# Kernel optimization log

Hardware: AMD Instinct MI355X
Metric: run time of the kernel (lower is better)

Reference implementation:

```python
import math
import jax, jax.numpy as jnp
import numpy as np

B, T, I, H = 32, 64, 256, 512
TAU = 20.0                      # tau_trace and membrane tau
DECAY = math.exp(-1.0 / TAU)    # exp trace decay (exp_convolve)
ALPHA = math.exp(-1.0 / TAU)    # leaky-integrator membrane decay
ETA = 0.1                       # Hebbian plasticity learning rate


def setup_inputs() -> dict:
    key = jax.random.key(0)
    kx, kw = jax.random.split(key)
    x = jax.random.normal(kx, (B, T, I), dtype=jnp.float32)
    # xavier_uniform with gain sqrt(2) ~ normal with matched std
    std = math.sqrt(2.0) * math.sqrt(2.0 / (2 * H + I))
    W = (jax.random.normal(kw, (2 * H, I), dtype=jnp.float32) * std)
    return {"x": x, "W": W}


def reference(x, W):
    """Write-mode (recall=False) forward of MemoryLayer.
    Returns (mem [B,H,H], keys [B,T,H], vals [B,T,H])."""
    h = W.shape[0] // 2
    b = x.shape[0]
    # i = linear(x, W): [B,T,2H], split into key/value drives
    i = jnp.einsum('bti,hi->bth', x, W)
    ik, iv = i[..., :h], i[..., h:]

    mem0 = jnp.zeros((b, h, h), x.dtype)
    z = jnp.zeros((b, h), x.dtype)

    def step(carry, inp):
        kv, vv, kt, vt, mem = carry
        ik_t, iv_t = inp
        # key neuron dynamics: leaky integration + tanh
        kv = ALPHA * kv + ik_t
        k = jnp.tanh(kv)
        # associative read: (key.unsqueeze(1) * mem).sum(2) == mem @ key
        ikv = 0.2 * jnp.einsum('bij,bj->bi', mem, k)
        # value neuron dynamics
        vv = ALPHA * vv + iv_t + ikv
        v = jnp.tanh(vv)
        # exp_convolve traces
        kt = DECAY * kt + (1.0 - DECAY) * k
        vt = DECAY * vt + (1.0 - DECAY) * v
        # Hebbian outer-product plasticity: delta_mem = eta * vt (x) kt
        mem = mem + ETA * jnp.einsum('bi,bj->bij', vt, kt)
        return (kv, vv, kt, vt, mem), (k, v)

    # scan over time (sequential recurrence), batch fully vectorized
    (kv, vv, kt, vt, mem), (ks, vs) = jax.lax.scan(
        step, (z, z, z, z, mem0),
        (jnp.swapaxes(ik, 0, 1), jnp.swapaxes(iv, 0, 1)))
    keys = jnp.swapaxes(ks, 0, 1)  # [B,T,H]
    vals = jnp.swapaxes(vs, 0, 1)  # [B,T,H]
    return mem, keys, vals
```

## Files before the change

kernel.cpp:

```cpp
#include <hip/hip_runtime.h>

#define B_ 32
#define T_ 64
#define I_ 256
#define H_ 512

static constexpr float ALPHA_F = 0.951229424500714f;
static constexpr float OMD_F   = 0.048770575499286f;
static constexpr float ETA_F   = 0.1f;
static constexpr float CSCALE  = 0.02f;

typedef __bf16 bf16x8 __attribute__((ext_vector_type(8)));
typedef float  f32x4  __attribute__((ext_vector_type(4)));

__device__ __forceinline__ float tanh_fast(float x) {
  float xc = fminf(fmaxf(x, -15.f), 15.f);
  float e = __expf(2.f * xc);
  return (e - 1.f) * __builtin_amdgcn_rcpf(e + 1.f);
}
__device__ __forceinline__ unsigned int f2bf(float f) {
  unsigned int u = __float_as_uint(f);
  u += 0x7fffu + ((u >> 16) & 1u);
  return u >> 16;
}
__device__ __forceinline__ void split8(const float* p, bf16x8& hi, bf16x8& lo) {
  float4 f0 = *reinterpret_cast<const float4*>(p);
  float4 f1 = *reinterpret_cast<const float4*>(p + 4);
  float f[8] = {f0.x, f0.y, f0.z, f0.w, f1.x, f1.y, f1.z, f1.w};
#pragma unroll
  for (int i = 0; i < 8; ++i) {
    __bf16 h = (__bf16)f[i];
    hi[i] = h;
    lo[i] = (__bf16)(f[i] - (float)h);
  }
}

template <int CTRL>
__device__ __forceinline__ float dpp_add(float x) {
  int mv = __builtin_amdgcn_update_dpp(0, __float_as_int(x), CTRL, 0xF, 0xF, true);
  return x + __int_as_float(mv);
}
__device__ __forceinline__ float wave_sum_dpp(float x) {
  x = dpp_add<0x111>(x);
  x = dpp_add<0x112>(x);
  x = dpp_add<0x114>(x);
  x = dpp_add<0x118>(x);
  x = dpp_add<0x142>(x);
  x = dpp_add<0x143>(x);
  return x;
}

__global__ __launch_bounds__(256) void proj_kscan(const float* __restrict__ x,
                                                  const float* __restrict__ W,
                                                  float* __restrict__ keys,
                                                  float* __restrict__ ktg,
                                                  ushort* __restrict__ ktb16T,
                                                  float* __restrict__ ivbuf) {
  __shared__ float scr[64][68];
  const int b  = blockIdx.x;
  const int n0 = blockIdx.y * 64;
  const int m0 = b * 64;
  const int tid = threadIdx.x;
  const int w = tid >> 6, l = tid & 63;
  const int lrow = l & 15, lk8 = (l >> 4) * 8;

  const float* xr = x + (size_t)(m0 + w * 16 + lrow) * I_ + lk8;
  const float* wr = W + (size_t)(n0 + lrow) * I_ + lk8;
  f32x4 acc[4] = {};
#pragma unroll
  for (int ks = 0; ks < 8; ++ks) {
    bf16x8 ah, al;
    split8(xr + ks * 32, ah, al);
#pragma unroll
    for (int jt = 0; jt < 4; ++jt) {
      bf16x8 bh, bl;
      split8(wr + (size_t)jt * 16 * I_ + ks * 32, bh, bl);
      acc[jt] = __builtin_amdgcn_mfma_f32_16x16x32_bf16(ah, bh, acc[jt], 0, 0, 0);
      acc[jt] = __builtin_amdgcn_mfma_f32_16x16x32_bf16(al, bh, acc[jt], 0, 0, 0);
      acc[jt] = __builtin_amdgcn_mfma_f32_16x16x32_bf16(ah, bl, acc[jt], 0, 0, 0);
    }
  }
  const int tr0 = (l >> 4) * 4, tc = lrow;

  if (n0 < 512) {
#pragma unroll
    for (int jt = 0; jt < 4; ++jt)
#pragma unroll
      for (int r = 0; r < 4; ++r)
        scr[w * 16 + tr0 + r][jt * 16 + tc] = acc[jt][r];
    __syncthreads();
    if (tid < 64) {
      float kv = 0.f, kt = 0.f;
      unsigned int kpk[32];
      float* ko  = keys + (size_t)b * T_ * H_ + n0 + tid;
      float* kto = ktg  + (size_t)b * T_ * H_ + n0 + tid;
#pragma unroll
      for (int t = 0; t < T_; ++t) {
        kv = ALPHA_F * kv + scr[t][tid];
        float k = tanh_fast(kv);
        kt = ALPHA_F * kt + OMD_F * k;
        ko[(size_t)t * H_]  = k;
        kto[(size_t)t * H_] = kt;
        unsigned int us = f2bf(kt);
        if ((t & 1) == 0) kpk[t >> 1] = us;
        else              kpk[t >> 1] |= us << 16;
      }
      ushort* kb = ktb16T + ((size_t)b * H_ + n0 + tid) * T_;
#pragma unroll
      for (int e = 0; e < 8; ++e)
        reinterpret_cast<uint4*>(kb)[e] =
            make_uint4(kpk[4 * e], kpk[4 * e + 1], kpk[4 * e + 2], kpk[4 * e + 3]);
    }
  } else {
    const int hv0 = n0 - 512;
#pragma unroll
    for (int jt = 0; jt < 4; ++jt)
#pragma unroll
      for (int r = 0; r < 4; ++r)
        ivbuf[((size_t)b * T_ + w * 16 + tr0 + r) * H_ + hv0 + jt * 16 + tc] = acc[jt][r];
  }
}

__global__ __launch_bounds__(512) void dots_kernel(const float* __restrict__ keys,
                                                   const float* __restrict__ ktg,
                                                   float* __restrict__ C) {
  const int b = blockIdx.y;
  const int t = blockIdx.x * 8 + (threadIdx.x >> 6);
  const int lane = threadIdx.x & 63;
  const float* krow = keys + ((size_t)b * T_ + t) * H_ + 4 * lane;
  float4 k0 = *reinterpret_cast<const float4*>(krow);
  float4 k1 = *reinterpret_cast<const float4*>(krow + 256);
  const float* tb = ktg + (size_t)b * T_ * H_ + 4 * lane;
  float* Cb = C + ((size_t)b * T_ + t) * T_;
#pragma unroll 8
  for (int s = 0; s < T_; ++s) {
    const float* ar = tb + (size_t)s * H_;
    float4 a0 = *reinterpret_cast<const float4*>(ar);
    float4 a1 = *reinterpret_cast<const float4*>(ar + 256);
    float p = a0.x * k0.x + a0.y * k0.y + a0.z * k0.z + a0.w * k0.w
            + a1.x * k1.x + a1.y * k1.y + a1.z * k1.z + a1.w * k1.w;
    p = wave_sum_dpp(p);
    if (lane == 63) Cb[s] = CSCALE * p;
  }
}

#define IVG(T) (((T) & 3) == 0 ? ivq[(T) >> 2].x : ((T) & 3) == 1 ? ivq[(T) >> 2].y \
              : ((T) & 3) == 2 ? ivq[(T) >> 2].z : ivq[(T) >> 2].w)
#define VQSET(T, val) do { \
    if (((T) & 3) == 0)      vqv[(T) >> 2].x = (val); \
    else if (((T) & 3) == 1) vqv[(T) >> 2].y = (val); \
    else if (((T) & 3) == 2) vqv[(T) >> 2].z = (val); \
    else                     vqv[(T) >> 2].w = (val); } while (0)

#define VSTEP(TT, CUR, NXT)                                                   \
  {                                                                           \
    if ((TT) + 1 < T_) {                                                      \
      _Pragma("unroll")                                                       \
      for (int q = 0; q < 16; ++q)                                            \
        NXT[q] = *reinterpret_cast<const float4*>(&Cs[(TT) + 1][4 * q]);      \
    }                                                                         \
    float p0 = 0.f, p1 = 0.f, p2 = 0.f, p3 = 0.f;                             \
    _Pragma("unroll")                                                         \
    for (int q = 0; q < 16; ++q) {                                            \
      p0 += CUR[q].x * vqv[q].x;                                              \
      p1 += CUR[q].y * vqv[q].y;                                              \
      p2 += CUR[q].z * vqv[q].z;                                              \
      p3 += CUR[q].w * vqv[q].w;                                              \
    }                                                                         \
    float ikv = (p0 + p1) + (p2 + p3);                                        \
    vv = ALPHA_F * vv + IVG(TT) + ikv;                                        \
    float v = tanh_fast(vv);                                                  \
    vt = ALPHA_F * vt + OMD_F * v;                                            \
    VQSET(TT, vt);                                                            \
    vo[(size_t)(TT) * H_] = v;                                                \
  }

#define VP2(T2) VSTEP(T2, ca, cbuf) VSTEP((T2) + 1, cbuf, ca)
#define VP8(T8) VP2(T8) VP2((T8) + 2) VP2((T8) + 4) VP2((T8) + 6)
#define IVLD(Q) { ivq[Q].x = pv[(size_t)(4 * (Q) + 0) * H_]; \
                  ivq[Q].y = pv[(size_t)(4 * (Q) + 1) * H_]; \
                  ivq[Q].z = pv[(size_t)(4 * (Q) + 2) * H_]; \
                  ivq[Q].w = pv[(size_t)(4 * (Q) + 3) * H_]; }

__global__ __launch_bounds__(64, 1) void vscan_kernel(const float* __restrict__ ivbuf,
                                                      const float* __restrict__ C,
                                                      float* __restrict__ vals,
                                                      ushort* __restrict__ vtb16T) {
  __shared__ float Cs[T_][T_];
  const int b    = blockIdx.x >> 3;
  const int lane = threadIdx.x;
  const int h    = ((blockIdx.x & 7) << 6) + lane;

  const float* Cb = C + (size_t)b * T_ * T_;
#pragma unroll
  for (int e = 0; e < 16; ++e)
    reinterpret_cast<float4*>(&Cs[0][0])[lane + (e << 6)] =
        reinterpret_cast<const float4*>(Cb)[lane + (e << 6)];

  const float* pv = ivbuf + (size_t)b * T_ * H_ + h;
  float* vo = vals + ((size_t)b * T_) * H_ + h;

  float4 ivq[16];
  IVLD(0)  IVLD(1)  IVLD(2)  IVLD(3)  IVLD(4)  IVLD(5)  IVLD(6)  IVLD(7)
  IVLD(8)  IVLD(9)  IVLD(10) IVLD(11) IVLD(12) IVLD(13) IVLD(14) IVLD(15)

  float vv = 0.f, vt = 0.f;
  float4 vqv[16];
#pragma unroll
  for (int q = 0; q < 16; ++q) vqv[q] = make_float4(0.f, 0.f, 0.f, 0.f);

  __syncthreads();

  float4 ca[16], cbuf[16];
#pragma unroll
  for (int q = 0; q < 16; ++q)
    ca[q] = *reinterpret_cast<const float4*>(&Cs[0][4 * q]);

  VP8(0) VP8(8) VP8(16) VP8(24) VP8(32) VP8(40) VP8(48) VP8(56)

  ushort* vb16 = vtb16T + ((size_t)b * H_ + h) * T_;
#pragma unroll
  for (int q = 0; q < 16; ++q) {
    unsigned int u0 = f2bf(vqv[q].x) | (f2bf(vqv[q].y) << 16);
    unsigned int u1 = f2bf(vqv[q].z) | (f2bf(vqv[q].w) << 16);
    reinterpret_cast<uint2*>(vb16)[q] = make_uint2(u0, u1);
  }
}

__global__ __launch_bounds__(256) void mem_mfma(const ushort* __restrict__ vtb16T,
                                                const ushort* __restrict__ ktb16T,
                                                float* __restrict__ mem) {
  const int b  = blockIdx.z;
  const int i0 = blockIdx.y * 64;
  const int j0 = blockIdx.x * 64;
  const int tid = threadIdx.x;
  const int w = tid >> 6, l = tid & 63;
  const int lrow = l & 15, lk8 = (l >> 4) * 8;

  const ushort* ar = vtb16T + ((size_t)b * H_ + i0 + w * 16 + lrow) * T_ + lk8;
  const ushort* br = ktb16T + ((size_t)b * H_ + j0 + lrow) * T_ + lk8;
  f32x4 acc[4] = {};
#pragma unroll
  for (int ks = 0; ks < 2; ++ks) {
    bf16x8 a = *reinterpret_cast<const bf16x8*>(ar + ks * 32);
#pragma unroll
    for (int jt = 0; jt < 4; ++jt) {
      bf16x8 bv = *reinterpret_cast<const bf16x8*>(br + (size_t)jt * 16 * T_ + ks * 32);
      acc[jt] = __builtin_amdgcn_mfma_f32_16x16x32_bf16(a, bv, acc[jt], 0, 0, 0);
    }
  }
  const int tr0 = (l >> 4) * 4, tc = lrow;
  float* mb = mem + (size_t)b * H_ * H_;
#pragma unroll
  for (int jt = 0; jt < 4; ++jt)
#pragma unroll
    for (int r = 0; r < 4; ++r)
      mb[((size_t)i0 + w * 16 + tr0 + r) * H_ + j0 + jt * 16 + tc] = ETA_F * acc[jt][r];
}

extern "C" void kernel_launch(void* const* d_in, const int* in_sizes, int n_in,
                              void* d_out, int out_size, void* d_ws, size_t ws_size,
                              hipStream_t stream) {
  const float* x = (const float*)d_in[0];
  const float* W = (const float*)d_in[1];
  float* out = (float*)d_out;
  float* mem  = out;
  float* keys = out + (size_t)B_ * H_ * H_;
  float* vals = keys + (size_t)B_ * T_ * H_;

  float*  ktg    = (float*)d_ws;
  float*  ivbuf  = ktg + (size_t)B_ * T_ * H_;
  ushort* ktb16T = (ushort*)(ivbuf + (size_t)B_ * T_ * H_);
  ushort* vtb16T = ktb16T + (size_t)B_ * H_ * T_;
  float*  Cbuf   = (float*)(vtb16T + (size_t)B_ * H_ * T_);

  proj_kscan<<<dim3(B_, 16), 256, 0, stream>>>(x, W, keys, ktg, ktb16T, ivbuf);
  dots_kernel<<<dim3(8, B_), 512, 0, stream>>>(keys, ktg, Cbuf);
  vscan_kernel<<<dim3(8 * B_), 64, 0, stream>>>(ivbuf, Cbuf, vals, vtb16T);
  mem_mfma<<<dim3(8, 8, B_), 256, 0, stream>>>(vtb16T, ktb16T, mem);
}
```

Baseline: 94.75 us.

## Fuse four stage kernels into one cooperative persistent kernel with grid syncs

Replaces the four separate launches (projection+key scan, dot products, value scan, mem outer product) with a single cooperative kernel of 256 blocks that loops over each stage's tasks and uses grid.sync between stages. This removes per-launch overhead and inter-kernel gaps. In exchange, the value-scan stage now runs on only 64 blocks of 4 waves each instead of 256 single-wave blocks, and grid-wide barriers add their own sync cost.

Result: slower. 205.1 us (+116.4%).

```diff
diff --git a/kernel.cpp b/kernel.cpp
--- a/kernel.cpp
+++ b/kernel.cpp
@@ -1,4 +1,7 @@
 #include <hip/hip_runtime.h>
+#include <hip/hip_cooperative_groups.h>
+
+namespace cg = cooperative_groups;
 
 #define B_ 32
 #define T_ 64
@@ -50,100 +53,7 @@
   return x;
 }
 
-__global__ __launch_bounds__(256) void proj_kscan(const float* __restrict__ x,
-                                                  const float* __restrict__ W,
-                                                  float* __restrict__ keys,
-                                                  float* __restrict__ ktg,
-                                                  ushort* __restrict__ ktb16T,
-                                                  float* __restrict__ ivbuf) {
-  __shared__ float scr[64][68];
-  const int b  = blockIdx.x;
-  const int n0 = blockIdx.y * 64;
-  const int m0 = b * 64;
-  const int tid = threadIdx.x;
-  const int w = tid >> 6, l = tid & 63;
-  const int lrow = l & 15, lk8 = (l >> 4) * 8;
-
-  const float* xr = x + (size_t)(m0 + w * 16 + lrow) * I_ + lk8;
-  const float* wr = W + (size_t)(n0 + lrow) * I_ + lk8;
-  f32x4 acc[4] = {};
-#pragma unroll
-  for (int ks = 0; ks < 8; ++ks) {
-    bf16x8 ah, al;
-    split8(xr + ks * 32, ah, al);
-#pragma unroll
-    for (int jt = 0; jt < 4; ++jt) {
-      bf16x8 bh, bl;
-      split8(wr + (size_t)jt * 16 * I_ + ks * 32, bh, bl);
-      acc[jt] = __builtin_amdgcn_mfma_f32_16x16x32_bf16(ah, bh, acc[jt], 0, 0, 0);
-      acc[jt] = __builtin_amdgcn_mfma_f32_16x16x32_bf16(al, bh, acc[jt], 0, 0, 0);
-      acc[jt] = __builtin_amdgcn_mfma_f32_16x16x32_bf16(ah, bl, acc[jt], 0, 0, 0);
-    }
-  }
-  const int tr0 = (l >> 4) * 4, tc = lrow;
-
-  if (n0 < 512) {
-#pragma unroll
-    for (int jt = 0; jt < 4; ++jt)
-#pragma unroll
-      for (int r = 0; r < 4; ++r)
-        scr[w * 16 + tr0 + r][jt * 16 + tc] = acc[jt][r];
-    __syncthreads();
-    if (tid < 64) {
-      float kv = 0.f, kt = 0.f;
-      unsigned int kpk[32];
-      float* ko  = keys + (size_t)b * T_ * H_ + n0 + tid;
-      float* kto = ktg  + (size_t)b * T_ * H_ + n0 + tid;
-#pragma unroll
-      for (int t = 0; t < T_; ++t) {
-        kv = ALPHA_F * kv + scr[t][tid];
-        float k = tanh_fast(kv);
-        kt = ALPHA_F * kt + OMD_F * k;
-        ko[(size_t)t * H_]  = k;
-        kto[(size_t)t * H_] = kt;
-        unsigned int us = f2bf(kt);
-        if ((t & 1) == 0) kpk[t >> 1] = us;
-        else              kpk[t >> 1] |= us << 16;
-      }
-      ushort* kb = ktb16T + ((size_t)b * H_ + n0 + tid) * T_;
-#pragma unroll
-      for (int e = 0; e < 8; ++e)
-        reinterpret_cast<uint4*>(kb)[e] =
-            make_uint4(kpk[4 * e], kpk[4 * e + 1], kpk[4 * e + 2], kpk[4 * e + 3]);
-    }
-  } else {
-    const int hv0 = n0 - 512;
-#pragma unroll
-    for (int jt = 0; jt < 4; ++jt)
-#pragma unroll
-      for (int r = 0; r < 4; ++r)
-        ivbuf[((size_t)b * T_ + w * 16 + tr0 + r) * H_ + hv0 + jt * 16 + tc] = acc[jt][r];
-  }
-}
-
-__global__ __launch_bounds__(512) void dots_kernel(const float* __restrict__ keys,
-                                                   const float* __restrict__ ktg,
-                                                   float* __restrict__ C) {
-  const int b = blockIdx.y;
-  const int t = blockIdx.x * 8 + (threadIdx.x >> 6);
-  const int lane = threadIdx.x & 63;
-  const float* krow = keys + ((size_t)b * T_ + t) * H_ + 4 * lane;
-  float4 k0 = *reinterpret_cast<const float4*>(krow);
-  float4 k1 = *reinterpret_cast<const float4*>(krow + 256);
-  const float* tb = ktg + (size_t)b * T_ * H_ + 4 * lane;
-  float* Cb = C + ((size_t)b * T_ + t) * T_;
-#pragma unroll 8
-  for (int s = 0; s < T_; ++s) {
-    const float* ar = tb + (size_t)s * H_;
-    float4 a0 = *reinterpret_cast<const float4*>(ar);
-    float4 a1 = *reinterpret_cast<const float4*>(ar + 256);
-    float p = a0.x * k0.x + a0.y * k0.y + a0.z * k0.z + a0.w * k0.w
-            + a1.x * k1.x + a1.y * k1.y + a1.z * k1.z + a1.w * k1.w;
-    p = wave_sum_dpp(p);
-    if (lane == 63) Cb[s] = CSCALE * p;
-  }
-}
-
+#define CSP(t) (smem + ((t) << 6))
 #define IVG(T) (((T) & 3) == 0 ? ivq[(T) >> 2].x : ((T) & 3) == 1 ? ivq[(T) >> 2].y \
               : ((T) & 3) == 2 ? ivq[(T) >> 2].z : ivq[(T) >> 2].w)
 #define VQSET(T, val) do { \
@@ -157,7 +67,7 @@
     if ((TT) + 1 < T_) {                                                      \
       _Pragma("unroll")                                                       \
       for (int q = 0; q < 16; ++q)                                            \
-        NXT[q] = *reinterpret_cast<const float4*>(&Cs[(TT) + 1][4 * q]);      \
+        NXT[q] = *reinterpret_cast<const float4*>(CSP((TT) + 1) + 4 * q);     \
     }                                                                         \
     float p0 = 0.f, p1 = 0.f, p2 = 0.f, p3 = 0.f;                             \
     _Pragma("unroll")                                                         \
@@ -182,80 +92,170 @@
                   ivq[Q].z = pv[(size_t)(4 * (Q) + 2) * H_]; \
                   ivq[Q].w = pv[(size_t)(4 * (Q) + 3) * H_]; }
 
-__global__ __launch_bounds__(64, 1) void vscan_kernel(const float* __restrict__ ivbuf,
-                                                      const float* __restrict__ C,
-                                                      float* __restrict__ vals,
-                                                      ushort* __restrict__ vtb16T) {
-  __shared__ float Cs[T_][T_];
-  const int b    = blockIdx.x >> 3;
-  const int lane = threadIdx.x;
-  const int h    = ((blockIdx.x & 7) << 6) + lane;
-
-  const float* Cb = C + (size_t)b * T_ * T_;
-#pragma unroll
-  for (int e = 0; e < 16; ++e)
-    reinterpret_cast<float4*>(&Cs[0][0])[lane + (e << 6)] =
-        reinterpret_cast<const float4*>(Cb)[lane + (e << 6)];
-
-  const float* pv = ivbuf + (size_t)b * T_ * H_ + h;
-  float* vo = vals + ((size_t)b * T_) * H_ + h;
-
-  float4 ivq[16];
-  IVLD(0)  IVLD(1)  IVLD(2)  IVLD(3)  IVLD(4)  IVLD(5)  IVLD(6)  IVLD(7)
-  IVLD(8)  IVLD(9)  IVLD(10) IVLD(11) IVLD(12) IVLD(13) IVLD(14) IVLD(15)
-
-  float vv = 0.f, vt = 0.f;
-  float4 vqv[16];
-#pragma unroll
-  for (int q = 0; q < 16; ++q) vqv[q] = make_float4(0.f, 0.f, 0.f, 0.f);
-
-  __syncthreads();
-
-  float4 ca[16], cbuf[16];
-#pragma unroll
-  for (int q = 0; q < 16; ++q)
-    ca[q] = *reinterpret_cast<const float4*>(&Cs[0][4 * q]);
-
-  VP8(0) VP8(8) VP8(16) VP8(24) VP8(32) VP8(40) VP8(48) VP8(56)
-
-  ushort* vb16 = vtb16T + ((size_t)b * H_ + h) * T_;
-#pragma unroll
-  for (int q = 0; q < 16; ++q) {
-    unsigned int u0 = f2bf(vqv[q].x) | (f2bf(vqv[q].y) << 16);
-    unsigned int u1 = f2bf(vqv[q].z) | (f2bf(vqv[q].w) << 16);
-    reinterpret_cast<uint2*>(vb16)[q] = make_uint2(u0, u1);
-  }
-}
-
-__global__ __launch_bounds__(256) void mem_mfma(const ushort* __restrict__ vtb16T,
-                                                const ushort* __restrict__ ktb16T,
-                                                float* __restrict__ mem) {
-  const int b  = blockIdx.z;
-  const int i0 = blockIdx.y * 64;
-  const int j0 = blockIdx.x * 64;
+__global__ __launch_bounds__(256, 1) void fused_kernel(
+    const float* __restrict__ x, const float* __restrict__ W,
+    float* __restrict__ keys, float* __restrict__ ktg,
+    ushort* __restrict__ ktb16T, float* __restrict__ ivbuf,
+    float* __restrict__ vals, ushort* __restrict__ vtb16T,
+    float* __restrict__ Cbuf, float* __restrict__ mem) {
+  cg::grid_group grid = cg::this_grid();
+  __shared__ __align__(16) float smem[64 * 68];
+  const int g = blockIdx.x;
   const int tid = threadIdx.x;
   const int w = tid >> 6, l = tid & 63;
   const int lrow = l & 15, lk8 = (l >> 4) * 8;
-
-  const ushort* ar = vtb16T + ((size_t)b * H_ + i0 + w * 16 + lrow) * T_ + lk8;
-  const ushort* br = ktb16T + ((size_t)b * H_ + j0 + lrow) * T_ + lk8;
-  f32x4 acc[4] = {};
-#pragma unroll
-  for (int ks = 0; ks < 2; ++ks) {
-    bf16x8 a = *reinterpret_cast<const bf16x8*>(ar + ks * 32);
-#pragma unroll
-    for (int jt = 0; jt < 4; ++jt) {
-      bf16x8 bv = *reinterpret_cast<const bf16x8*>(br + (size_t)jt * 16 * T_ + ks * 32);
-      acc[jt] = __builtin_amdgcn_mfma_f32_16x16x32_bf16(a, bv, acc[jt], 0, 0, 0);
-    }
-  }
   const int tr0 = (l >> 4) * 4, tc = lrow;
-  float* mb = mem + (size_t)b * H_ * H_;
-#pragma unroll
-  for (int jt = 0; jt < 4; ++jt)
-#pragma unroll
-    for (int r = 0; r < 4; ++r)
-      mb[((size_t)i0 + w * 16 + tr0 + r) * H_ + j0 + jt * 16 + tc] = ETA_F * acc[jt][r];
+
+#pragma unroll
+  for (int it = 0; it < 2; ++it) {
+    const int tau = g + it * 256;
+    const int b  = tau >> 4;
+    const int n0 = (tau & 15) * 64;
+    const int m0 = b * 64;
+    __syncthreads();
+    const float* xr = x + (size_t)(m0 + w * 16 + lrow) * I_ + lk8;
+    const float* wr = W + (size_t)(n0 + lrow) * I_ + lk8;
+    f32x4 acc[4] = {};
+#pragma unroll
+    for (int ks = 0; ks < 8; ++ks) {
+      bf16x8 ah, al;
+      split8(xr + ks * 32, ah, al);
+#pragma unroll
+      for (int jt = 0; jt < 4; ++jt) {
+        bf16x8 bh, bl;
+        split8(wr + (size_t)jt * 16 * I_ + ks * 32, bh, bl);
+        acc[jt] = __builtin_amdgcn_mfma_f32_16x16x32_bf16(ah, bh, acc[jt], 0, 0, 0);
+        acc[jt] = __builtin_amdgcn_mfma_f32_16x16x32_bf16(al, bh, acc[jt], 0, 0, 0);
+        acc[jt] = __builtin_amdgcn_mfma_f32_16x16x32_bf16(ah, bl, acc[jt], 0, 0, 0);
+      }
+    }
+    if (n0 < 512) {
+#pragma unroll
+      for (int jt = 0; jt < 4; ++jt)
+#pragma unroll
+        for (int r = 0; r < 4; ++r)
+          smem[(w * 16 + tr0 + r) * 68 + jt * 16 + tc] = acc[jt][r];
+      __syncthreads();
+      if (tid < 64) {
+        float kv = 0.f, kt = 0.f;
+        unsigned int kpk[32];
+        float* ko  = keys + (size_t)b * T_ * H_ + n0 + tid;
+        float* kto = ktg  + (size_t)b * T_ * H_ + n0 + tid;
+#pragma unroll
+        for (int t = 0; t < T_; ++t) {
+          kv = ALPHA_F * kv + smem[t * 68 + tid];
+          float k = tanh_fast(kv);
+          kt = ALPHA_F * kt + OMD_F * k;
+          ko[(size_t)t * H_]  = k;
+          kto[(size_t)t * H_] = kt;
+          unsigned int us = f2bf(kt);
+          if ((t & 1) == 0) kpk[t >> 1] = us;
+          else              kpk[t >> 1] |= us << 16;
+        }
+        ushort* kb = ktb16T + ((size_t)b * H_ + n0 + tid) * T_;
+#pragma unroll
+        for (int e = 0; e < 8; ++e)
+          reinterpret_cast<uint4*>(kb)[e] =
+              make_uint4(kpk[4 * e], kpk[4 * e + 1], kpk[4 * e + 2], kpk[4 * e + 3]);
+      }
+    } else {
+      const int hv0 = n0 - 512;
+#pragma unroll
+      for (int jt = 0; jt < 4; ++jt)
+#pragma unroll
+        for (int r = 0; r < 4; ++r)
+          ivbuf[((size_t)b * T_ + w * 16 + tr0 + r) * H_ + hv0 + jt * 16 + tc] = acc[jt][r];
+    }
+  }
+  grid.sync();
+
+#pragma unroll
+  for (int it = 0; it < 2; ++it) {
+    const int task = it * 1024 + g * 4 + w;
+    const int b = task >> 6, t = task & 63;
+    const float* krow = keys + ((size_t)b * T_ + t) * H_ + 4 * l;
+    float4 k0 = *reinterpret_cast<const float4*>(krow);
+    float4 k1 = *reinterpret_cast<const float4*>(krow + 256);
+    const float* tb = ktg + (size_t)b * T_ * H_ + 4 * l;
+    float* Cb = Cbuf + ((size_t)b * T_ + t) * T_;
+#pragma unroll 8
+    for (int s = 0; s < T_; ++s) {
+      const float* ar = tb + (size_t)s * H_;
+      float4 a0 = *reinterpret_cast<const float4*>(ar);
+      float4 a1 = *reinterpret_cast<const float4*>(ar + 256);
+      float p = a0.x * k0.x + a0.y * k0.y + a0.z * k0.z + a0.w * k0.w
+              + a1.x * k1.x + a1.y * k1.y + a1.z * k1.z + a1.w * k1.w;
+      p = wave_sum_dpp(p);
+      if (l == 63) Cb[s] = CSCALE * p;
+    }
+  }
+  grid.sync();
+
+  if (g < 64) {
+    const int b = g >> 1;
+#pragma unroll
+    for (int e = 0; e < 4; ++e)
+      reinterpret_cast<float4*>(smem)[tid + (e << 8)] =
+          reinterpret_cast<const float4*>(Cbuf + (size_t)b * T_ * T_)[tid + (e << 8)];
+    __syncthreads();
+
+    const int hb = ((g & 1) << 2) + w;
+    const int h  = (hb << 6) + l;
+    const float* pv = ivbuf + (size_t)b * T_ * H_ + h;
+    float* vo = vals + ((size_t)b * T_) * H_ + h;
+
+    float4 ivq[16];
+    IVLD(0)  IVLD(1)  IVLD(2)  IVLD(3)  IVLD(4)  IVLD(5)  IVLD(6)  IVLD(7)
+    IVLD(8)  IVLD(9)  IVLD(10) IVLD(11) IVLD(12) IVLD(13) IVLD(14) IVLD(15)
+
+    float vv = 0.f, vt = 0.f;
+    float4 vqv[16];
+#pragma unroll
+    for (int q = 0; q < 16; ++q) vqv[q] = make_float4(0.f, 0.f, 0.f, 0.f);
+
+    float4 ca[16], cbuf[16];
+#pragma unroll
+    for (int q = 0; q < 16; ++q)
+      ca[q] = *reinterpret_cast<const float4*>(CSP(0) + 4 * q);
+
+    VP8(0) VP8(8) VP8(16) VP8(24) VP8(32) VP8(40) VP8(48) VP8(56)
+
+    ushort* vb16 = vtb16T + ((size_t)b * H_ + h) * T_;
+#pragma unroll
+    for (int q = 0; q < 16; ++q) {
+      unsigned int u0 = f2bf(vqv[q].x) | (f2bf(vqv[q].y) << 16);
+      unsigned int u1 = f2bf(vqv[q].z) | (f2bf(vqv[q].w) << 16);
+      reinterpret_cast<uint2*>(vb16)[q] = make_uint2(u0, u1);
+    }
+  }
+  grid.sync();
+
+#pragma unroll
+  for (int it = 0; it < 8; ++it) {
+    const int task = it * 256 + g;
+    const int b   = task >> 6;
+    const int rem = task & 63;
+    const int i0 = (rem >> 3) << 6;
+    const int j0 = (rem & 7) << 6;
+    const ushort* ar = vtb16T + ((size_t)b * H_ + i0 + w * 16 + lrow) * T_ + lk8;
+    const ushort* br = ktb16T + ((size_t)b * H_ + j0 + lrow) * T_ + lk8;
+    f32x4 acc[4] = {};
+#pragma unroll
+    for (int ks = 0; ks < 2; ++ks) {
+      bf16x8 a = *reinterpret_cast<const bf16x8*>(ar + ks * 32);
+#pragma unroll
+      for (int jt = 0; jt < 4; ++jt) {
+        bf16x8 bv = *reinterpret_cast<const bf16x8*>(br + (size_t)jt * 16 * T_ + ks * 32);
+        acc[jt] = __builtin_amdgcn_mfma_f32_16x16x32_bf16(a, bv, acc[jt], 0, 0, 0);
+      }
+    }
+    float* mb = mem + (size_t)b * H_ * H_;
+#pragma unroll
+    for (int jt = 0; jt < 4; ++jt)
+#pragma unroll
+      for (int r = 0; r < 4; ++r)
+        mb[((size_t)i0 + w * 16 + tr0 + r) * H_ + j0 + jt * 16 + tc] = ETA_F * acc[jt][r];
+  }
 }
 
 extern "C" void kernel_launch(void* const* d_in, const int* in_sizes, int n_in,
@@ -274,8 +274,8 @@
   ushort* vtb16T = ktb16T + (size_t)B_ * H_ * T_;
   float*  Cbuf   = (float*)(vtb16T + (size_t)B_ * H_ * T_);
 
-  proj_kscan<<<dim3(B_, 16), 256, 0, stream>>>(x, W, keys, ktg, ktb16T, ivbuf);
-  dots_kernel<<<dim3(8, B_), 512, 0, stream>>>(keys, ktg, Cbuf);
-  vscan_kernel<<<dim3(8 * B_), 64, 0, stream>>>(ivbuf, Cbuf, vals, vtb16T);
-  mem_mfma<<<dim3(8, 8, B_), 256, 0, stream>>>(vtb16T, ktb16T, mem);
-}
+  void* kargs[] = {(void*)&x, (void*)&W, (void*)&keys, (void*)&ktg, (void*)&ktb16T,
+                   (void*)&ivbuf, (void*)&vals, (void*)&vtb16T, (void*)&Cbuf, (void*)&mem};
+  (void)hipLaunchCooperativeKernel((const void*)fused_kernel, dim3(256), dim3(256),
+                                   kargs, 0, stream);
+}
```
